# Kernel tuning notes

Measured on AMD Instinct MI355X. Metric: run time of the kernel, lower is better.

Reference implementation:

```python
import jax, jax.numpy as jnp
import numpy as np

EPS = 1e-7

def _logmap0(x):
    # Poincare ball (c=1) log map at the origin: artanh(||x||) * x/||x||
    n = jnp.linalg.norm(x, axis=-1, keepdims=True)
    n = jnp.clip(n, EPS, 1.0 - EPS)
    return jnp.arctanh(n) * x / n

def _expmap0(v):
    # Poincare ball (c=1) exp map at the origin: tanh(||v||) * v/||v||
    n = jnp.maximum(jnp.linalg.norm(v, axis=-1, keepdims=True), EPS)
    return jnp.tanh(n) * v / n

def setup_inputs() -> dict:
    N, E, DIN, DOUT = 100000, 1000000, 512, 512
    key = jax.random.key(0)
    k1, k2, k3, k4, k5, k6 = jax.random.split(key, 6)
    g = jax.random.normal(k1, (N, DIN), jnp.float32)
    # points strictly inside the unit ball (valid Poincare coordinates)
    r = 0.9 * jax.random.uniform(k2, (N, 1), jnp.float32)
    x = g / jnp.maximum(jnp.linalg.norm(g, axis=-1, keepdims=True), 1e-6) * r
    src = jax.random.randint(k3, (E,), 0, N)
    dst = jax.random.randint(k4, (E,), 0, N)
    W = jax.random.normal(k5, (DOUT, DIN), jnp.float32) / np.sqrt(DIN).astype(np.float32)
    b = jax.random.normal(k6, (DOUT,), jnp.float32) * 0.01
    return {"x": x, "src": src, "dst": dst, "W": W, "b": b}

def reference(x, src, dst, W, b):
    N = x.shape[0]
    tangent = _logmap0(x)                      # [N, din]
    h = tangent @ W.T + b                      # [N, dout] (nn.Linear)
    # DGL update_all(copy_u, mean): mean over incoming edges per dst node;
    # zero-in-degree nodes get 0 (DGL convention).
    sums = jax.ops.segment_sum(h[src], dst, num_segments=N)          # [N, dout]
    deg = jax.ops.segment_sum(jnp.ones_like(dst, dtype=h.dtype), dst, num_segments=N)
    neigh = sums / jnp.maximum(deg, 1.0)[:, None]
    return _expmap0(neigh)
```

## Files before the change

### kernel.cpp

```cpp
#include <hip/hip_runtime.h>
#include <stdint.h>

#define DIN 512
#define DOUT 512
#define HB 256
#define BKT_SH 7

typedef short bf16x8 __attribute__((ext_vector_type(8)));
typedef float floatx4 __attribute__((ext_vector_type(4)));
typedef float f32x4 __attribute__((ext_vector_type(4)));

static __device__ __forceinline__ ushort f2bf(float f) {
  uint32_t u = __float_as_uint(f);
  u += 0x7FFFu + ((u >> 16) & 1u);
  return (ushort)(u >> 16);
}

static __device__ __forceinline__ void gload16(const ushort* g, ushort* l) {
  __builtin_amdgcn_global_load_lds(
      (const __attribute__((address_space(1))) unsigned int*)g,
      (__attribute__((address_space(3))) unsigned int*)l, 16, 0, 0);
}

__global__ __launch_bounds__(256) void fused1_kernel(
    const float* __restrict__ x, ushort* __restrict__ tanb,
    const float* __restrict__ W, ushort* __restrict__ Wbf,
    const int* __restrict__ dst, int* __restrict__ ghist, int N, int E, int NB) {
  __shared__ int hist[1024];
  int bid = blockIdx.x;
  int tx = threadIdx.x;
  if (bid < HB) {
    for (int i = tx; i < NB; i += 256) hist[i] = 0;
    __syncthreads();
    int EPB = (E + HB - 1) / HB;
    int e0 = bid * EPB;
    int e1 = e0 + EPB; if (e1 > E) e1 = E;
    for (int e = e0 + tx; e < e1; e += 256)
      atomicAdd(&hist[dst[e] >> BKT_SH], 1);
    __syncthreads();
    for (int b = tx; b < NB; b += 256)
      ghist[b * HB + bid] = hist[b];
    return;
  }
  bid -= HB;
  int logB = (N + 3) >> 2;
  if (bid < logB) {
    int row = bid * 4 + (tx >> 6);
    if (row >= N) return;
    int lane = tx & 63;
    const f32x4* xr = (const f32x4*)(x + (size_t)row * DIN);
    f32x4 v0 = __builtin_nontemporal_load(xr + lane * 2);
    f32x4 v1 = __builtin_nontemporal_load(xr + lane * 2 + 1);
    float ss = v0[0]*v0[0] + v0[1]*v0[1] + v0[2]*v0[2] + v0[3]*v0[3] +
               v1[0]*v1[0] + v1[1]*v1[1] + v1[2]*v1[2] + v1[3]*v1[3];
#pragma unroll
    for (int m = 32; m >= 1; m >>= 1) ss += __shfl_xor(ss, m, 64);
    float n = sqrtf(ss);
    float nc = fminf(fmaxf(n, 1e-7f), 1.0f - 1e-7f);
    float scale = atanhf(nc) / nc;
    union { ushort s[8]; uint4 v; } o;
    o.s[0] = f2bf(v0[0] * scale); o.s[1] = f2bf(v0[1] * scale);
    o.s[2] = f2bf(v0[2] * scale); o.s[3] = f2bf(v0[3] * scale);
    o.s[4] = f2bf(v1[0] * scale); o.s[5] = f2bf(v1[1] * scale);
    o.s[6] = f2bf(v1[2] * scale); o.s[7] = f2bf(v1[3] * scale);
    *(uint4*)(tanb + (size_t)row * DIN + lane * 8) = o.v;
    return;
  }
  bid -= logB;
  int i = bid * 1024 + tx * 4;
  float4 w4 = *(const float4*)(W + i);
  ushort4 o4;
  o4.x = f2bf(w4.x); o4.y = f2bf(w4.y); o4.z = f2bf(w4.z); o4.w = f2bf(w4.w);
  *(ushort4*)(Wbf + i) = o4;
}

__global__ __launch_bounds__(256) void scan1_kernel(const int* __restrict__ in,
                                                    int* __restrict__ outp,
                                                    int* __restrict__ bsum, int L) {
  __shared__ int s[256];
  int tx = threadIdx.x;
  int i = blockIdx.x * 256 + tx;
  int v = (i < L) ? in[i] : 0;
  s[tx] = v;
  __syncthreads();
#pragma unroll
  for (int d = 1; d < 256; d <<= 1) {
    int t = (tx >= d) ? s[tx - d] : 0;
    __syncthreads();
    s[tx] += t;
    __syncthreads();
  }
  if (i < L) outp[i] = s[tx] - v;
  if (tx == 255) bsum[blockIdx.x] = s[255];
}

__global__ __launch_bounds__(1024) void scan2_kernel(int* __restrict__ bsum, int B) {
  __shared__ int s[1024];
  int tx = threadIdx.x;
  int v = (tx < B) ? bsum[tx] : 0;
  s[tx] = v;
  __syncthreads();
#pragma unroll
  for (int d = 1; d < 1024; d <<= 1) {
    int t = (tx >= d) ? s[tx - d] : 0;
    __syncthreads();
    s[tx] += t;
    __syncthreads();
  }
  if (tx < B) bsum[tx] = s[tx] - v;
}

__global__ __launch_bounds__(256) void scan3_kernel(int* __restrict__ outp,
                                                    const int* __restrict__ bsum, int L) {
  int i = blockIdx.x * 256 + threadIdx.x;
  if (i < L) outp[i] += bsum[blockIdx.x];
}

__global__ __launch_bounds__(256) void cscatter_kernel(
    const int* __restrict__ src, const int* __restrict__ dst,
    const int* __restrict__ gscan, uint32_t* __restrict__ cs, int E, int NB) {
  __shared__ int lcur[1024];
  int j = blockIdx.x, tx = threadIdx.x;
  for (int b = tx; b < NB; b += 256) lcur[b] = gscan[b * HB + j];
  __syncthreads();
  int EPB = (E + HB - 1) / HB;
  int e0 = j * EPB;
  int e1 = e0 + EPB; if (e1 > E) e1 = E;
  for (int e = e0 + tx; e < e1; e += 256) {
    int d = dst[e];
    int p = atomicAdd(&lcur[d >> BKT_SH], 1);
    cs[p] = ((uint32_t)src[e] << BKT_SH) | (uint32_t)(d & ((1 << BKT_SH) - 1));
  }
}

__global__ __launch_bounds__(256) void gemmfill_kernel(
    const ushort* __restrict__ A, const ushort* __restrict__ Bw,
    const float* __restrict__ bias, ushort* __restrict__ Hb, int M,
    const int* __restrict__ gscan, const uint32_t* __restrict__ cs,
    int* __restrict__ adj, int* __restrict__ offs, int E, int NB, int FB) {
  __shared__ __align__(16) ushort smem[16384];
  int bid = blockIdx.x;
  int tid = threadIdx.x;
  if (bid < FB) {
    int b = bid;
    int S = gscan[b * HB];
    int T = (b + 1 < NB) ? gscan[(b + 1) * HB] : E;
    int base = b << BKT_SH;
    int* sdeg = (int*)smem;
    int* scur = sdeg + 128;
    int* sscn = scur + 128;
    if (tid < 128) sdeg[tid] = 0;
    __syncthreads();
    for (int e = S + tid; e < T; e += 256)
      atomicAdd(&sdeg[cs[e] & 127], 1);
    __syncthreads();
    if (tid < 128) sscn[tid] = sdeg[tid];
    __syncthreads();
#pragma unroll
    for (int d = 1; d < 128; d <<= 1) {
      int t = (tid >= d && tid < 128) ? sscn[tid - d] : 0;
      __syncthreads();
      if (tid < 128) sscn[tid] += t;
      __syncthreads();
    }
    if (tid < 128) {
      int excl = sscn[tid] - sdeg[tid];
      scur[tid] = excl;
      int node = base + tid;
      int Nn = NB << BKT_SH;  (void)Nn;
      if (node < M) offs[node] = S + excl;
    }
    if (tid == 0 && b == NB - 1) offs[M] = E;
    __syncthreads();
    for (int e = S + tid; e < T; e += 256) {
      uint32_t v = cs[e];
      int p = atomicAdd(&scur[v & 127], 1);
      adj[S + p] = (int)(v >> BKT_SH);
    }
    return;
  }
  bid -= FB;
  int TB = (int)gridDim.x - FB;
  int q = TB >> 3, r = TB & 7;
  int xcd = bid & 7, off = bid >> 3;
  int w = (xcd < r) ? xcd * (q + 1) + off : r * (q + 1) + (xcd - r) * q + off;
  int n0 = (w & 3) * 128;
  int m0 = (w >> 2) * 128;

  ushort* As = smem;
  ushort* Bs = smem + 8192;
  int wave = tid >> 6, lane = tid & 63;
  int wm = (wave >> 1) * 64, wn = (wave & 1) * 64;
  int fr = lane & 15, fq = lane >> 4;
  int rsub = lane >> 3;
  int ksw = ((lane & 7) ^ rsub) * 8;

  floatx4 acc[4][4] = {};

  for (int k0 = 0; k0 < DIN; k0 += 64) {
#pragma unroll
    for (int i = 0; i < 4; i++) {
      int g = wave * 4 + i;
      int ra = g * 8 + rsub;
      int gm = m0 + ra; if (gm >= M) gm = M - 1;
      gload16(A + (size_t)gm * DIN + k0 + ksw, As + g * 512);
      gload16(Bw + (size_t)(n0 + ra) * DIN + k0 + ksw, Bs + g * 512);
    }
    __syncthreads();
#pragma unroll
    for (int kk = 0; kk < 2; kk++) {
      bf16x8 af[4], bg[4];
#pragma unroll
      for (int t = 0; t < 4; t++) {
        int ra = wm + t * 16 + fr;
        af[t] = *(const bf16x8*)(As + ra * 64 + (((kk * 4 + fq) ^ (ra & 7)) << 3));
        int rb = wn + t * 16 + fr;
        bg[t] = *(const bf16x8*)(Bs + rb * 64 + (((kk * 4 + fq) ^ (rb & 7)) << 3));
      }
#pragma unroll
      for (int mt = 0; mt < 4; mt++)
#pragma unroll
        for (int nt = 0; nt < 4; nt++)
          acc[mt][nt] = __builtin_amdgcn_mfma_f32_16x16x32_bf16(
              af[mt], bg[nt], acc[mt][nt], 0, 0, 0);
    }
    __syncthreads();
  }

  int rq = fq * 4;
#pragma unroll
  for (int nt = 0; nt < 4; nt++) {
    int col = wn + nt * 16 + fr;
    float bb = bias[n0 + col];
    int c16 = col >> 3;
#pragma unroll
    for (int mt = 0; mt < 4; mt++) {
#pragma unroll
      for (int rr = 0; rr < 4; rr++) {
        int row = wm + mt * 16 + rq + rr;
        smem[row * 128 + (((c16 ^ (row & 7)) << 3) | (col & 7))] =
            f2bf(acc[mt][nt][rr] + bb);
      }
    }
  }
  __syncthreads();
#pragma unroll
  for (int p = 0; p < 8; p++) {
    int idx = p * 256 + tid;
    int row = idx >> 4, cc = idx & 15;
    uint4 v = *(const uint4*)(smem + row * 128 + ((cc ^ (row & 7)) << 3));
    int gm = m0 + row;
    if (gm < M) *(uint4*)(Hb + (size_t)gm * DOUT + n0 + cc * 8) = v;
  }
}

static __device__ __forceinline__ void accum8(float* acc, uint4 v) {
  acc[0] += __uint_as_float(v.x << 16); acc[1] += __uint_as_float(v.x & 0xFFFF0000u);
  acc[2] += __uint_as_float(v.y << 16); acc[3] += __uint_as_float(v.y & 0xFFFF0000u);
  acc[4] += __uint_as_float(v.z << 16); acc[5] += __uint_as_float(v.z & 0xFFFF0000u);
  acc[6] += __uint_as_float(v.w << 16); acc[7] += __uint_as_float(v.w & 0xFFFF0000u);
}

__global__ __launch_bounds__(256) void aggregate_kernel(const ushort* __restrict__ hb,
                                                        const int* __restrict__ adj,
                                                        const int* __restrict__ offs,
                                                        float* __restrict__ out, int N) {
  int row = blockIdx.x * 4 + (threadIdx.x >> 6);
  if (row >= N) return;
  int lane = threadIdx.x & 63;
  int base = offs[row];
  int dg = offs[row + 1] - base;
  float acc[8] = {0.f, 0.f, 0.f, 0.f, 0.f, 0.f, 0.f, 0.f};
  int j = 0;
  for (; j + 8 <= dg; j += 8) {
    int av = adj[base + j + (lane & 7)];
    uint4 v[8];
#pragma unroll
    for (int qq = 0; qq < 8; qq++) {
      int s = __builtin_amdgcn_readlane(av, qq);
      v[qq] = *(const uint4*)(hb + (size_t)s * DOUT + lane * 8);
    }
#pragma unroll
    for (int qq = 0; qq < 8; qq++) accum8(acc, v[qq]);
  }
  for (; j + 4 <= dg; j += 4) {
    int av = adj[base + j + (lane & 3)];
    uint4 v[4];
#pragma unroll
    for (int qq = 0; qq < 4; qq++) {
      int s = __builtin_amdgcn_readlane(av, qq);
      v[qq] = *(const uint4*)(hb + (size_t)s * DOUT + lane * 8);
    }
#pragma unroll
    for (int qq = 0; qq < 4; qq++) accum8(acc, v[qq]);
  }
  for (; j < dg; j++) {
    int s = __builtin_amdgcn_readfirstlane(adj[base + j]);
    uint4 a = *(const uint4*)(hb + (size_t)s * DOUT + lane * 8);
    accum8(acc, a);
  }
  float inv = 1.0f / fmaxf((float)dg, 1.0f);
  float ss = 0.f;
#pragma unroll
  for (int k = 0; k < 8; k++) ss += acc[k] * acc[k];
#pragma unroll
  for (int m = 32; m >= 1; m >>= 1) ss += __shfl_xor(ss, m, 64);
  float n = fmaxf(inv * sqrtf(ss), 1e-7f);
  float sc = tanhf(n) / n * inv;
  f32x4 o0 = {acc[0] * sc, acc[1] * sc, acc[2] * sc, acc[3] * sc};
  f32x4 o1 = {acc[4] * sc, acc[5] * sc, acc[6] * sc, acc[7] * sc};
  float* orow = out + (size_t)row * DOUT + lane * 8;
  __builtin_nontemporal_store(o0, (f32x4*)orow);
  __builtin_nontemporal_store(o1, (f32x4*)(orow + 4));
}

extern "C" void kernel_launch(void* const* d_in, const int* in_sizes, int n_in,
                              void* d_out, int out_size, void* d_ws, size_t ws_size,
                              hipStream_t stream) {
  const float* x = (const float*)d_in[0];
  const int* src = (const int*)d_in[1];
  const int* dst = (const int*)d_in[2];
  const float* W = (const float*)d_in[3];
  const float* b = (const float*)d_in[4];
  int N = in_sizes[0] / DIN;
  int E = in_sizes[1];
  float* out = (float*)d_out;

  int NB = (N + 127) >> BKT_SH;
  int L = NB * HB;

  char* ws = (char*)d_ws;
  size_t off = 0;
  ushort* Wbf = (ushort*)(ws + off); off += (size_t)DOUT * DIN * 2;
  ushort* tanb = (ushort*)(ws + off); off += (size_t)N * DIN * 2;
  ushort* hb = (ushort*)(ws + off); off += (size_t)N * DIN * 2;
  off = (off + 255) & ~(size_t)255;
  int* offs = (int*)(ws + off); off += (size_t)(N + 1) * 4;
  off = (off + 255) & ~(size_t)255;
  int* ghist = (int*)(ws + off); off += (size_t)L * 4;
  off = (off + 255) & ~(size_t)255;
  int* gscan = (int*)(ws + off); off += (size_t)L * 4;
  off = (off + 255) & ~(size_t)255;
  int* bsum = (int*)(ws + off); off += 1024 * 4;
  off = (off + 255) & ~(size_t)255;
  uint32_t* cs = (uint32_t*)(ws + off); off += (size_t)E * 4;
  off = (off + 255) & ~(size_t)255;
  int* adj = (int*)(ws + off); off += (size_t)E * 4;

  int logB = (N + 3) >> 2;
  int wB = (DOUT * DIN) / 1024;
  fused1_kernel<<<HB + logB + wB, 256, 0, stream>>>(x, tanb, W, Wbf, dst, ghist,
                                                    N, E, NB);

  scan1_kernel<<<NB, 256, 0, stream>>>(ghist, gscan, bsum, L);
  scan2_kernel<<<1, 1024, 0, stream>>>(bsum, NB);
  scan3_kernel<<<NB, 256, 0, stream>>>(gscan, bsum, L);

  cscatter_kernel<<<HB, 256, 0, stream>>>(src, dst, gscan, cs, E, NB);

  int MB = (N + 127) >> 7;
  int FB = NB;
  gemmfill_kernel<<<FB + 4 * MB, 256, 0, stream>>>(tanb, Wbf, b, hb, N,
                                                   gscan, cs, adj, offs, E, NB, FB);

  aggregate_kernel<<<(N + 3) / 4, 256, 0, stream>>>(hb, adj, offs, out, N);
}
```

Measured before the change: 590.5 us.

## Fold scan fixup into consumers and aggregate two rows per wavefront

Removes the scan3 pass by adding the per-bucket block sums directly where the scanned histogram is consumed, in the scatter and fill stages, so one kernel launch goes away. The aggregation kernel now gives each wavefront two destination rows. It preloads up to 64 neighbour indices per row into lanes and interleaves the gathers of both rows, which puts more independent loads in flight. Rows with degree above 64 fall back to a serial loop. The cost is more registers per wave and extra predicated branching.

```diff
diff --git a/kernel.cpp b/kernel.cpp
--- a/kernel.cpp
+++ b/kernel.cpp
@@ -110,18 +110,13 @@
   if (tx < B) bsum[tx] = s[tx] - v;
 }
 
-__global__ __launch_bounds__(256) void scan3_kernel(int* __restrict__ outp,
-                                                    const int* __restrict__ bsum, int L) {
-  int i = blockIdx.x * 256 + threadIdx.x;
-  if (i < L) outp[i] += bsum[blockIdx.x];
-}
-
 __global__ __launch_bounds__(256) void cscatter_kernel(
     const int* __restrict__ src, const int* __restrict__ dst,
-    const int* __restrict__ gscan, uint32_t* __restrict__ cs, int E, int NB) {
+    const int* __restrict__ gscan, const int* __restrict__ bsum,
+    uint32_t* __restrict__ cs, int E, int NB) {
   __shared__ int lcur[1024];
   int j = blockIdx.x, tx = threadIdx.x;
-  for (int b = tx; b < NB; b += 256) lcur[b] = gscan[b * HB + j];
+  for (int b = tx; b < NB; b += 256) lcur[b] = gscan[b * HB + j] + bsum[b];
   __syncthreads();
   int EPB = (E + HB - 1) / HB;
   int e0 = j * EPB;
@@ -136,15 +131,15 @@
 __global__ __launch_bounds__(256) void gemmfill_kernel(
     const ushort* __restrict__ A, const ushort* __restrict__ Bw,
     const float* __restrict__ bias, ushort* __restrict__ Hb, int M,
-    const int* __restrict__ gscan, const uint32_t* __restrict__ cs,
+    const int* __restrict__ bsum, const uint32_t* __restrict__ cs,
     int* __restrict__ adj, int* __restrict__ offs, int E, int NB, int FB) {
   __shared__ __align__(16) ushort smem[16384];
   int bid = blockIdx.x;
   int tid = threadIdx.x;
   if (bid < FB) {
     int b = bid;
-    int S = gscan[b * HB];
-    int T = (b + 1 < NB) ? gscan[(b + 1) * HB] : E;
+    int S = bsum[b];
+    int T = (b + 1 < NB) ? bsum[b + 1] : E;
     int base = b << BKT_SH;
     int* sdeg = (int*)smem;
     int* scur = sdeg + 128;
@@ -167,7 +162,6 @@
       int excl = sscn[tid] - sdeg[tid];
       scur[tid] = excl;
       int node = base + tid;
-      int Nn = NB << BKT_SH;  (void)Nn;
       if (node < M) offs[node] = S + excl;
     }
     if (tid == 0 && b == NB - 1) offs[M] = E;
@@ -261,44 +255,8 @@
   acc[6] += __uint_as_float(v.w << 16); acc[7] += __uint_as_float(v.w & 0xFFFF0000u);
 }
 
-__global__ __launch_bounds__(256) void aggregate_kernel(const ushort* __restrict__ hb,
-                                                        const int* __restrict__ adj,
-                                                        const int* __restrict__ offs,
-                                                        float* __restrict__ out, int N) {
-  int row = blockIdx.x * 4 + (threadIdx.x >> 6);
-  if (row >= N) return;
-  int lane = threadIdx.x & 63;
-  int base = offs[row];
-  int dg = offs[row + 1] - base;
-  float acc[8] = {0.f, 0.f, 0.f, 0.f, 0.f, 0.f, 0.f, 0.f};
-  int j = 0;
-  for (; j + 8 <= dg; j += 8) {
-    int av = adj[base + j + (lane & 7)];
-    uint4 v[8];
-#pragma unroll
-    for (int qq = 0; qq < 8; qq++) {
-      int s = __builtin_amdgcn_readlane(av, qq);
-      v[qq] = *(const uint4*)(hb + (size_t)s * DOUT + lane * 8);
-    }
-#pragma unroll
-    for (int qq = 0; qq < 8; qq++) accum8(acc, v[qq]);
-  }
-  for (; j + 4 <= dg; j += 4) {
-    int av = adj[base + j + (lane & 3)];
-    uint4 v[4];
-#pragma unroll
-    for (int qq = 0; qq < 4; qq++) {
-      int s = __builtin_amdgcn_readlane(av, qq);
-      v[qq] = *(const uint4*)(hb + (size_t)s * DOUT + lane * 8);
-    }
-#pragma unroll
-    for (int qq = 0; qq < 4; qq++) accum8(acc, v[qq]);
-  }
-  for (; j < dg; j++) {
-    int s = __builtin_amdgcn_readfirstlane(adj[base + j]);
-    uint4 a = *(const uint4*)(hb + (size_t)s * DOUT + lane * 8);
-    accum8(acc, a);
-  }
+static __device__ __forceinline__ void finish_row(float* acc, int dg, int row,
+                                                  int lane, float* __restrict__ out) {
   float inv = 1.0f / fmaxf((float)dg, 1.0f);
   float ss = 0.f;
 #pragma unroll
@@ -312,6 +270,61 @@
   float* orow = out + (size_t)row * DOUT + lane * 8;
   __builtin_nontemporal_store(o0, (f32x4*)orow);
   __builtin_nontemporal_store(o1, (f32x4*)(orow + 4));
+}
+
+__global__ __launch_bounds__(256) void aggregate_kernel(const ushort* __restrict__ hb,
+                                                        const int* __restrict__ adj,
+                                                        const int* __restrict__ offs,
+                                                        float* __restrict__ out, int N) {
+  int wid = blockIdx.x * 4 + (threadIdx.x >> 6);
+  int r0 = wid * 2;
+  if (r0 >= N) return;
+  int r1 = r0 + 1;
+  int has1 = (r1 < N);
+  int lane = threadIdx.x & 63;
+  int b0 = offs[r0];
+  int e0 = offs[r0 + 1];
+  int e1 = has1 ? offs[r0 + 2] : e0;
+  int dg0 = e0 - b0;
+  int dg1 = e1 - e0;
+  int c0 = dg0 < 64 ? dg0 : 64;
+  int c1 = dg1 < 64 ? dg1 : 64;
+  int av0 = (lane < c0) ? adj[b0 + lane] : 0;
+  int av1 = (lane < c1) ? adj[e0 + lane] : 0;
+  float acc0[8] = {0.f, 0.f, 0.f, 0.f, 0.f, 0.f, 0.f, 0.f};
+  float acc1[8] = {0.f, 0.f, 0.f, 0.f, 0.f, 0.f, 0.f, 0.f};
+  int mx = c0 > c1 ? c0 : c1;
+  for (int j = 0; j < mx; j += 8) {
+    uint4 v0[8], v1[8];
+    int n0 = c0 - j; n0 = n0 < 0 ? 0 : (n0 > 8 ? 8 : n0);
+    int n1 = c1 - j; n1 = n1 < 0 ? 0 : (n1 > 8 ? 8 : n1);
+#pragma unroll
+    for (int q = 0; q < 8; q++)
+      if (q < n0) {
+        int s = __builtin_amdgcn_readlane(av0, j + q);
+        v0[q] = *(const uint4*)(hb + (size_t)s * DOUT + lane * 8);
+      }
+#pragma unroll
+    for (int q = 0; q < 8; q++)
+      if (q < n1) {
+        int s = __builtin_amdgcn_readlane(av1, j + q);
+        v1[q] = *(const uint4*)(hb + (size_t)s * DOUT + lane * 8);
+      }
+#pragma unroll
+    for (int q = 0; q < 8; q++) if (q < n0) accum8(acc0, v0[q]);
+#pragma unroll
+    for (int q = 0; q < 8; q++) if (q < n1) accum8(acc1, v1[q]);
+  }
+  for (int j = 64; j < dg0; j++) {
+    int s = __builtin_amdgcn_readfirstlane(adj[b0 + j]);
+    accum8(acc0, *(const uint4*)(hb + (size_t)s * DOUT + lane * 8));
+  }
+  for (int j = 64; j < dg1; j++) {
+    int s = __builtin_amdgcn_readfirstlane(adj[e0 + j]);
+    accum8(acc1, *(const uint4*)(hb + (size_t)s * DOUT + lane * 8));
+  }
+  finish_row(acc0, dg0, r0, lane, out);
+  if (has1) finish_row(acc1, dg1, r1, lane, out);
 }
 
 extern "C" void kernel_launch(void* const* d_in, const int* in_sizes, int n_in,
@@ -354,14 +367,13 @@
 
   scan1_kernel<<<NB, 256, 0, stream>>>(ghist, gscan, bsum, L);
   scan2_kernel<<<1, 1024, 0, stream>>>(bsum, NB);
-  scan3_kernel<<<NB, 256, 0, stream>>>(gscan, bsum, L);
-
-  cscatter_kernel<<<HB, 256, 0, stream>>>(src, dst, gscan, cs, E, NB);
+
+  cscatter_kernel<<<HB, 256, 0, stream>>>(src, dst, gscan, bsum, cs, E, NB);
 
   int MB = (N + 127) >> 7;
   int FB = NB;
   gemmfill_kernel<<<FB + 4 * MB, 256, 0, stream>>>(tanb, Wbf, b, hb, N,
-                                                   gscan, cs, adj, offs, E, NB, FB);
-
-  aggregate_kernel<<<(N + 3) / 4, 256, 0, stream>>>(hb, adj, offs, out, N);
-}
+                                                   bsum, cs, adj, offs, E, NB, FB);
+
+  aggregate_kernel<<<(N + 7) / 8, 256, 0, stream>>>(hb, adj, offs, out, N);
+}
```

Result: no change. 590.0 us (-0.1%).
